# Performance work log

Measured on AMD Instinct MI355X. Metric: run time of the kernel, lower is better.

The kernel has to match this reference:

```python
import jax, jax.numpy as jnp
import numpy as np

D_AU, D_LM, D_GZ = 35, 196, 2   # au = 235 - 196 - 2 - 2
D, H = 128, 4
HD = D // H
LN_EPS = 1e-5


def setup_inputs() -> dict:
    key = jax.random.key(0)
    ks = jax.random.split(key, 12)
    s = lambda k, shape: jax.random.normal(k, shape, jnp.float32) * 0.02
    return {
        "video_feat": jax.random.normal(ks[0], (32, 4096, 235), jnp.float32),
        "au_w": s(ks[1], (D, D_AU)), "au_b": jnp.zeros((D,), jnp.float32),
        "lm_w": s(ks[2], (D, D_LM)), "lm_b": jnp.zeros((D,), jnp.float32),
        "gz_w": s(ks[3], (D, D_GZ)), "gz_b": jnp.zeros((D,), jnp.float32),
        "in_w": s(ks[4], (3 * D, D)), "in_b": jnp.zeros((3 * D,), jnp.float32),
        "out_w": s(ks[5], (D, D)), "out_b": jnp.zeros((D,), jnp.float32),
        "ln_g": jnp.ones((D,), jnp.float32), "ln_b": jnp.zeros((D,), jnp.float32),
        "w_w": s(ks[6], (1, D)), "w_b": jnp.zeros((1,), jnp.float32),
    }


def reference(video_feat, au_w, au_b, lm_w, lm_b, gz_w, gz_b,
              in_w, in_b, out_w, out_b, ln_g, ln_b, w_w, w_b):
    B, N, _ = video_feat.shape
    # split OpenFace3 features into semantic groups (meta dims unused, as in torch)
    au = video_feat[..., :D_AU]
    lm = video_feat[..., D_AU:D_AU + D_LM]
    gz = video_feat[..., D_AU + D_LM:D_AU + D_LM + D_GZ]
    au_h = au @ au_w.T + au_b
    lm_h = lm @ lm_w.T + lm_b
    gz_h = gz @ gz_w.T + gz_b
    tok = jnp.stack([au_h, lm_h, gz_h], axis=2).reshape(B * N, 3, D)  # (BN,3,D)

    # nn.MultiheadAttention (batch_first): packed in_proj then out_proj
    qkv = tok @ in_w.T + in_b                      # (BN,3,3D)
    q, k, v = jnp.split(qkv, 3, axis=-1)
    def heads(x):
        return x.reshape(-1, 3, H, HD).transpose(0, 2, 1, 3)  # (BN,H,3,HD)
    q, k, v = heads(q), heads(k), heads(v)
    scores = jnp.einsum('bhqd,bhkd->bhqk', q, k) / jnp.sqrt(jnp.float32(HD))
    attn = jax.nn.softmax(scores, axis=-1)
    o = jnp.einsum('bhqk,bhkd->bhqd', attn, v)
    o = o.transpose(0, 2, 1, 3).reshape(-1, 3, D)
    attn_out = o @ out_w.T + out_b

    # residual + LayerNorm
    x = attn_out + tok
    mu = x.mean(axis=-1, keepdims=True)
    var = x.var(axis=-1, keepdims=True)
    x = (x - mu) * jax.lax.rsqrt(var + LN_EPS) * ln_g + ln_b

    # softmax-weighted pooling over the 3 group tokens
    w = jax.nn.softmax((x @ w_w.T + w_b)[..., 0], axis=-1)  # (BN,3)
    fused = jnp.einsum('bt,btd->bd', w, x)
    return fused.reshape(B, N, D)
```

## Files before the change

### kernel.cpp

```cpp
#include <hip/hip_runtime.h>
#include <hip/hip_bf16.h>

typedef __hip_bfloat16 bf16;
typedef short  frag_t __attribute__((ext_vector_type(8)));
typedef float  f4     __attribute__((ext_vector_type(4)));
typedef unsigned short us8 __attribute__((ext_vector_type(8)));
typedef unsigned short us4 __attribute__((ext_vector_type(4)));

#define NPOS (32 * 4096)
#define CIN  235

#define W1F 0
#define W2F 98304
#define W3F 147456
#define FRAG_TOTAL 163840
#define FP32_OFF_BYTES (FRAG_TOTAL * 2)
#define F_BIAS 0
#define F_INB  384
#define F_OUTB 768
#define F_LNG  896
#define F_LNB  1024
#define F_GW   1152
#define F_BW   1280
#define F_SGW  1281
#define WS2_BYTES (FP32_OFF_BYTES + 1282 * 4)

__device__ __forceinline__ float b2f(bf16 x) { return __bfloat162float(x); }
__device__ __forceinline__ unsigned short f2b(float v) {
    bf16 h = __float2bfloat16(v);
    return __builtin_bit_cast(unsigned short, h);
}
__device__ __forceinline__ float b2fr(unsigned short u) {
    return __bfloat162float(__builtin_bit_cast(bf16, u));
}
__device__ __forceinline__ bool probe_is_f32(const void* ln_g) {
    return *(const unsigned int*)ln_g == 0x3F800000u;
}
__device__ __forceinline__ float ldany(const void* p, int i, bool f32) {
    return f32 ? ((const float*)p)[i] : b2f(((const bf16*)p)[i]);
}
template<typename IT> __device__ __forceinline__ float ldv(const void* p, size_t i);
template<> __device__ __forceinline__ float ldv<float>(const void* p, size_t i) { return ((const float*)p)[i]; }
template<> __device__ __forceinline__ float ldv<bf16>(const void* p, size_t i)  { return b2f(((const bf16*)p)[i]); }
template<typename IT> __device__ __forceinline__ void stv(void* p, size_t i, float v);
template<> __device__ __forceinline__ void stv<float>(void* p, size_t i, float v) { ((float*)p)[i] = v; }
template<> __device__ __forceinline__ void stv<bf16>(void* p, size_t i, float v)  { ((bf16*)p)[i] = __float2bfloat16(v); }

__device__ __forceinline__ int tok_idx(int row, int col) {
    return row * 128 + (col ^ ((row & 7) << 3));
}
__device__ __forceinline__ int qk_idx(int row, int col) {
    return row * 264 + col;
}
__device__ __forceinline__ int sx_idx(int row, int col) {
    return row * 132 + col;
}

__global__ __launch_bounds__(256) void kprep(
    const void* __restrict__ au_w, const void* __restrict__ au_b,
    const void* __restrict__ lm_w, const void* __restrict__ lm_b,
    const void* __restrict__ gz_w, const void* __restrict__ gz_b,
    const void* __restrict__ in_w, const void* __restrict__ in_b,
    const void* __restrict__ out_w, const void* __restrict__ out_b,
    const void* __restrict__ ln_g, const void* __restrict__ ln_b,
    const void* __restrict__ w_w, const void* __restrict__ w_b,
    void* __restrict__ ws)
{
    const bool f32 = probe_is_f32(ln_g);
    unsigned short* wf = (unsigned short*)ws;
    float* wsf = (float*)((char*)ws + FP32_OFF_BYTES);

    if (blockIdx.x == 645) {
        if (threadIdx.x < 64) {
            int lane = threadIdx.x;
            float bw = 0.f, sg = 0.f;
            for (int j = lane; j < 128; j += 64) {
                float wwj = ldany(w_w, j, f32);
                bw += ldany(ln_b, j, f32) * wwj;
                sg += ldany(ln_g, j, f32) * wwj;
            }
#pragma unroll
            for (int off = 32; off >= 1; off >>= 1) {
                bw += __shfl_down(bw, off);
                sg += __shfl_down(sg, off);
            }
            if (lane == 0) {
                wsf[F_BW]  = bw + ldany(w_b, 0, f32);
                wsf[F_SGW] = sg;
            }
        }
        return;
    }

    int idx = blockIdx.x * 256 + threadIdx.x;
    if (idx < FRAG_TOTAL) {
        float val = 0.f;
        if (idx < W2F) {
            int r = idx, j = r & 7, lane = (r >> 3) & 63, q = r >> 9;
            int tn = q % 24, ks = q / 24;
            int k = ks * 32 + (lane >> 4) * 8 + j;
            int c = tn * 16 + (lane & 15);
            int t = c >> 7, jo = c & 127;
            if (t == 0 && k < 35)                   val = ldany(au_w, jo * 35 + k, f32);
            else if (t == 1 && k >= 35 && k < 231)  val = ldany(lm_w, jo * 196 + (k - 35), f32);
            else if (t == 2 && k >= 231 && k < 233) val = ldany(gz_w, jo * 2 + (k - 231), f32);
        } else if (idx < W3F) {
            int r = idx - W2F, j = r & 7, lane = (r >> 3) & 63, q = r >> 9;
            int tn = q % 24, ks = q / 24;
            int k = ks * 32 + (lane >> 4) * 8 + j;
            int c = tn * 16 + (lane & 15);
            val = ldany(in_w, c * 128 + k, f32);
        } else {
            int r = idx - W3F, j = r & 7, lane = (r >> 3) & 63, q = r >> 9;
            int tn = q & 7, ks = q >> 3;
            int k = ks * 32 + (lane >> 4) * 8 + j;
            int c = tn * 16 + (lane & 15);
            val = ldany(out_w, c * 128 + k, f32);
        }
        wf[idx] = f2b(val);
    } else if (idx < FRAG_TOTAL + 1280) {
        int i2 = idx - FRAG_TOTAL;
        float v;
        if (i2 < 384) {
            int t = i2 >> 7, jo = i2 & 127;
            const void* b = (t == 0) ? au_b : ((t == 1) ? lm_b : gz_b);
            v = ldany(b, jo, f32);
        } else if (i2 < 768)  v = ldany(in_b,  i2 - 384, f32);
        else if   (i2 < 896)  v = ldany(out_b, i2 - 768, f32);
        else if   (i2 < 1024) v = ldany(ln_g,  i2 - 896, f32);
        else if   (i2 < 1152) v = ldany(ln_b,  i2 - 1024, f32);
        else                  v = ldany(ln_g, i2 - 1152, f32) * ldany(w_w, i2 - 1152, f32);
        wsf[i2] = v;
    }
}

__global__ __launch_bounds__(256, 4) void sga_mfma(
    const void* __restrict__ vf, const void* __restrict__ ln_g,
    const void* __restrict__ ws, void* __restrict__ out)
{
    const bool f32 = probe_is_f32(ln_g);
    const int tid = threadIdx.x;
    const int w = tid >> 6, lane = tid & 63, quad = lane >> 4, l16 = lane & 15;
    const int p0 = blockIdx.x * 16;

    const frag_t* wfr = (const frag_t*)ws;
    const float*  wsf = (const float*)((const char*)ws + FP32_OFF_BYTES);

    __shared__ __align__(16) unsigned char u_buf[25344];
    __shared__ __align__(16) unsigned short s_tok[6144];
    __shared__ float s_ar[576];
    __shared__ float s_mu[48], s_rs[48], s_w[16][3];

    unsigned short (*s_vf)[264] = (unsigned short(*)[264])u_buf;
    unsigned short* s_qkf = (unsigned short*)u_buf;
    float*          s_xf  = (float*)u_buf;

    for (int z = tid; z < 384; z += 256) {
        int rz = z / 24, cz = z - rz * 24;
        s_vf[rz][233 + cz] = 0;
    }
    if (f32) {
        const float* src = (const float*)vf + (size_t)p0 * CIN;
#pragma unroll
        for (int it = 0; it < 4; ++it) {
            int idx = it * 256 + tid;
            if (idx < 940) {
                float4 vv = *(const float4*)(src + idx * 4);
                int e = idx * 4;
                int r = e / 235, c = e - r * 235;
#pragma unroll
                for (int j = 0; j < 4; ++j) {
                    int rj = r, cj = c + j;
                    if (cj >= 235) { rj++; cj -= 235; }
                    if (cj < 233) s_vf[rj][cj] = f2b(((const float*)&vv)[j]);
                }
            }
        }
    } else {
        const unsigned short* src = (const unsigned short*)vf + (size_t)p0 * CIN;
#pragma unroll
        for (int it = 0; it < 2; ++it) {
            int idx = it * 256 + tid;
            if (idx < 470) {
                us8 vv = *(const us8*)(src + idx * 8);
                int e = idx * 8;
                int r = e / 235, c = e - r * 235;
#pragma unroll
                for (int j = 0; j < 8; ++j) {
                    int rj = r, cj = c + j;
                    if (cj >= 235) { rj++; cj -= 235; }
                    if (cj < 233) s_vf[rj][cj] = vv[j];
                }
            }
        }
    }
    __syncthreads();

    {
        frag_t a[8];
#pragma unroll
        for (int ks = 0; ks < 8; ++ks)
            a[ks] = *(const frag_t*)&s_vf[l16][ks * 32 + quad * 8];
#pragma unroll
        for (int tn6 = 0; tn6 < 6; ++tn6) {
            int tn = w * 6 + tn6;
            f4 acc = {0.f, 0.f, 0.f, 0.f};
#pragma unroll
            for (int ks = 0; ks < 8; ++ks) {
                frag_t b = wfr[W1F / 8 + (ks * 24 + tn) * 64 + lane];
                acc = __builtin_amdgcn_mfma_f32_16x16x32_bf16(b, a[ks], acc, 0, 0, 0);
            }
            int c0 = tn * 16 + quad * 4;
            int t = c0 >> 7, jo0 = c0 & 127;
            float4 bias = *(const float4*)&wsf[F_BIAS + c0];
            us4 pv;
            pv[0] = f2b(acc[0] + bias.x); pv[1] = f2b(acc[1] + bias.y);
            pv[2] = f2b(acc[2] + bias.z); pv[3] = f2b(acc[3] + bias.w);
            *(us4*)&s_tok[tok_idx(l16 * 3 + t, jo0)] = pv;
        }
    }
    __syncthreads();

    {
        frag_t a[3][4];
#pragma unroll
        for (int rt = 0; rt < 3; ++rt)
#pragma unroll
            for (int ks = 0; ks < 4; ++ks)
                a[rt][ks] = *(const frag_t*)&s_tok[tok_idx(rt * 16 + l16, ks * 32 + quad * 8)];
#pragma unroll
        for (int tn4 = 0; tn4 < 4; ++tn4) {
            int tn = w * 4 + tn4;
            f4 acc[3];
#pragma unroll
            for (int rt = 0; rt < 3; ++rt) acc[rt] = (f4){0.f, 0.f, 0.f, 0.f};
#pragma unroll
            for (int ks = 0; ks < 4; ++ks) {
                frag_t b = wfr[W2F / 8 + (ks * 24 + tn) * 64 + lane];
#pragma unroll
                for (int rt = 0; rt < 3; ++rt)
                    acc[rt] = __builtin_amdgcn_mfma_f32_16x16x32_bf16(b, a[rt][ks], acc[rt], 0, 0, 0);
            }
            int c0 = tn * 16 + quad * 4;
            float4 bias = *(const float4*)&wsf[F_INB + c0];
#pragma unroll
            for (int rt = 0; rt < 3; ++rt) {
                us4 pv;
                pv[0] = f2b(acc[rt][0] + bias.x); pv[1] = f2b(acc[rt][1] + bias.y);
                pv[2] = f2b(acc[rt][2] + bias.z); pv[3] = f2b(acc[rt][3] + bias.w);
                *(us4*)&s_qkf[qk_idx(rt * 16 + l16, c0)] = pv;
            }
        }
    }
    __syncthreads();

    {
        const int h = w;
        frag_t qf[3], kf[3];
#pragma unroll
        for (int t = 0; t < 3; ++t) {
            qf[t] = *(const frag_t*)&s_qkf[qk_idx(l16 * 3 + t, h * 32 + quad * 8)];
            kf[t] = *(const frag_t*)&s_qkf[qk_idx(l16 * 3 + t, 128 + h * 32 + quad * 8)];
        }
        float dv[3][3];
        const int rr = l16 & 3;
#pragma unroll
        for (int t = 0; t < 3; ++t)
#pragma unroll
            for (int k = 0; k < 3; ++k) {
                f4 acc = {0.f, 0.f, 0.f, 0.f};
                acc = __builtin_amdgcn_mfma_f32_16x16x32_bf16(qf[t], kf[k], acc, 0, 0, 0);
                float d = acc[0];
                d = rr == 1 ? acc[1] : d;
                d = rr == 2 ? acc[2] : d;
                d = rr == 3 ? acc[3] : d;
                dv[t][k] = d;
            }
        if ((l16 >> 2) == quad) {
            const float scale = 0.17677669529663687f;
            int base0 = (l16 * 4 + h) * 9;
#pragma unroll
            for (int t = 0; t < 3; ++t) {
                float s0 = dv[t][0] * scale, s1 = dv[t][1] * scale, s2 = dv[t][2] * scale;
                float m = fmaxf(s0, fmaxf(s1, s2));
                float e0 = __expf(s0 - m), e1 = __expf(s1 - m), e2 = __expf(s2 - m);
                float inv = 1.f / (e0 + e1 + e2);
                s_ar[base0 + t * 3 + 0] = e0 * inv;
                s_ar[base0 + t * 3 + 1] = e1 * inv;
                s_ar[base0 + t * 3 + 2] = e2 * inv;
            }
        }
    }
    __syncthreads();

    {
        frag_t a[3][4];
#pragma unroll
        for (int rt = 0; rt < 3; ++rt)
#pragma unroll
            for (int ks = 0; ks < 4; ++ks)
                a[rt][ks] = *(const frag_t*)&s_tok[tok_idx(rt * 16 + l16, ks * 32 + quad * 8)];
#pragma unroll
        for (int tn2 = 0; tn2 < 2; ++tn2) {
            int tn = 16 + w * 2 + tn2;
            f4 acc[3];
#pragma unroll
            for (int rt = 0; rt < 3; ++rt) acc[rt] = (f4){0.f, 0.f, 0.f, 0.f};
#pragma unroll
            for (int ks = 0; ks < 4; ++ks) {
                frag_t b = wfr[W2F / 8 + (ks * 24 + tn) * 64 + lane];
#pragma unroll
                for (int rt = 0; rt < 3; ++rt)
                    acc[rt] = __builtin_amdgcn_mfma_f32_16x16x32_bf16(b, a[rt][ks], acc[rt], 0, 0, 0);
            }
            int c0 = tn * 16 + quad * 4;
            float4 bias = *(const float4*)&wsf[F_INB + c0];
#pragma unroll
            for (int rt = 0; rt < 3; ++rt) {
                us4 pv;
                pv[0] = f2b(acc[rt][0] + bias.x); pv[1] = f2b(acc[rt][1] + bias.y);
                pv[2] = f2b(acc[rt][2] + bias.z); pv[3] = f2b(acc[rt][3] + bias.w);
                *(us4*)&s_qkf[qk_idx(rt * 16 + l16, c0 - 256)] = pv;
            }
        }
    }
    __syncthreads();

    for (int u = 0; u < 3; ++u) {
        int unit = u * 256 + tid;
        int row = unit >> 4, c8 = (unit & 15) << 3;
        int p = row / 3, t = row - p * 3, h = c8 >> 5;
        int base = (p * 4 + h) * 9 + t * 3;
        float a0 = s_ar[base], a1 = s_ar[base + 1], a2 = s_ar[base + 2];
        us8 v0 = *(const us8*)&s_qkf[qk_idx(p * 3 + 0, c8)];
        us8 v1 = *(const us8*)&s_qkf[qk_idx(p * 3 + 1, c8)];
        us8 v2 = *(const us8*)&s_qkf[qk_idx(p * 3 + 2, c8)];
        us8 o;
#pragma unroll
        for (int jj = 0; jj < 8; ++jj)
            o[jj] = f2b(a0 * b2fr(v0[jj]) + a1 * b2fr(v1[jj]) + a2 * b2fr(v2[jj]));
        *(us8*)&s_qkf[qk_idx(row, 128 + c8)] = o;
    }
    __syncthreads();

    frag_t of[3][4];
#pragma unroll
    for (int rt = 0; rt < 3; ++rt)
#pragma unroll
        for (int ks = 0; ks < 4; ++ks)
            of[rt][ks] = *(const frag_t*)&s_qkf[qk_idx(rt * 16 + l16, 128 + ks * 32 + quad * 8)];
    __syncthreads();

    {
#pragma unroll
        for (int tn2 = 0; tn2 < 2; ++tn2) {
            int tn = w * 2 + tn2;
            f4 acc[3];
#pragma unroll
            for (int rt = 0; rt < 3; ++rt) acc[rt] = (f4){0.f, 0.f, 0.f, 0.f};
#pragma unroll
            for (int ks = 0; ks < 4; ++ks) {
                frag_t b = wfr[W3F / 8 + (ks * 8 + tn) * 64 + lane];
#pragma unroll
                for (int rt = 0; rt < 3; ++rt)
                    acc[rt] = __builtin_amdgcn_mfma_f32_16x16x32_bf16(b, of[rt][ks], acc[rt], 0, 0, 0);
            }
            int c0 = tn * 16 + quad * 4;
            float4 ob4 = *(const float4*)&wsf[F_OUTB + c0];
#pragma unroll
            for (int rt = 0; rt < 3; ++rt) {
                int row = rt * 16 + l16;
                us4 tv = *(const us4*)&s_tok[tok_idx(row, c0)];
                float4 xv;
                xv.x = acc[rt][0] + ob4.x + b2fr(tv[0]);
                xv.y = acc[rt][1] + ob4.y + b2fr(tv[1]);
                xv.z = acc[rt][2] + ob4.z + b2fr(tv[2]);
                xv.w = acc[rt][3] + ob4.w + b2fr(tv[3]);
                *(float4*)&s_xf[sx_idx(row, c0)] = xv;
            }
        }
    }
    __syncthreads();

    if (tid < 192) {
        int row = tid >> 2, part = tid & 3;
        float s = 0.f, ss = 0.f, sg = 0.f;
#pragma unroll
        for (int cc = 0; cc < 8; ++cc) {
            float4 xv = *(const float4*)&s_xf[sx_idx(row, part * 32 + cc * 4)];
            int cg = F_GW + part * 32 + cc * 4;
            s  += xv.x + xv.y + xv.z + xv.w;
            ss += xv.x * xv.x + xv.y * xv.y + xv.z * xv.z + xv.w * xv.w;
            sg += xv.x * wsf[cg] + xv.y * wsf[cg + 1] + xv.z * wsf[cg + 2] + xv.w * wsf[cg + 3];
        }
        int b = (row * 4 + part) * 3;
        s_ar[b] = s; s_ar[b + 1] = ss; s_ar[b + 2] = sg;
    }
    __syncthreads();
    if (tid < 64) {
        float lg = 0.f;
        if (lane < 48) {
            float s = 0.f, ss = 0.f, sg = 0.f;
#pragma unroll
            for (int part = 0; part < 4; ++part) {
                int b = (lane * 4 + part) * 3;
                s += s_ar[b]; ss += s_ar[b + 1]; sg += s_ar[b + 2];
            }
            float mu  = s * (1.f / 128.f);
            float var = ss * (1.f / 128.f) - mu * mu;
            float rs  = rsqrtf(var + 1e-5f);
            s_mu[lane] = mu; s_rs[lane] = rs;
            lg = wsf[F_BW] + rs * (sg - mu * wsf[F_SGW]);
        }
        float l0 = __shfl(lg, 3 * lane);
        float l1 = __shfl(lg, 3 * lane + 1);
        float l2 = __shfl(lg, 3 * lane + 2);
        if (lane < 16) {
            float m = fmaxf(l0, fmaxf(l1, l2));
            float e0 = __expf(l0 - m), e1 = __expf(l1 - m), e2 = __expf(l2 - m);
            float inv = 1.f / (e0 + e1 + e2);
            s_w[lane][0] = e0 * inv; s_w[lane][1] = e1 * inv; s_w[lane][2] = e2 * inv;
        }
    }
    __syncthreads();

    {
#pragma unroll
        for (int it = 0; it < 2; ++it) {
            int task = it * 256 + tid;
            int p = task >> 5, cg = (task & 31) * 4;
            int row0 = p * 3;
            float c0 = s_w[p][0] * s_rs[row0];
            float c1 = s_w[p][1] * s_rs[row0 + 1];
            float c2 = s_w[p][2] * s_rs[row0 + 2];
            float C  = c0 * s_mu[row0] + c1 * s_mu[row0 + 1] + c2 * s_mu[row0 + 2];
            float4 g = *(const float4*)&wsf[F_LNG + cg];
            float4 b = *(const float4*)&wsf[F_LNB + cg];
            float4 x0 = *(const float4*)&s_xf[sx_idx(row0, cg)];
            float4 x1 = *(const float4*)&s_xf[sx_idx(row0 + 1, cg)];
            float4 x2 = *(const float4*)&s_xf[sx_idx(row0 + 2, cg)];
            float4 f;
            f.x = (c0 * x0.x + c1 * x1.x + c2 * x2.x - C) * g.x + b.x;
            f.y = (c0 * x0.y + c1 * x1.y + c2 * x2.y - C) * g.y + b.y;
            f.z = (c0 * x0.z + c1 * x1.z + c2 * x2.z - C) * g.z + b.z;
            f.w = (c0 * x0.w + c1 * x1.w + c2 * x2.w - C) * g.w + b.w;
            size_t o0 = (size_t)(p0 + p) * 128 + cg;
            if (f32) {
                *(float4*)((float*)out + o0) = f;
            } else {
                us4 pv;
                pv[0] = f2b(f.x); pv[1] = f2b(f.y); pv[2] = f2b(f.z); pv[3] = f2b(f.w);
                *(us4*)((bf16*)out + o0) = pv;
            }
        }
    }
}

#define P 4
struct SmemFB {
    float vf[P][233];
    alignas(16) float tok[P][128][4];
    float qkv[P][3][384];
    float att[P][4][3][3];
    alignas(16) float o[P][128][4];
    float x[P][3][128];
    float red[P][3][2];
    float w[P][4];
};

template<typename IT>
__device__ void sga_fb_body(SmemFB& s,
    const void* vf, const void* au_w, const void* au_b, const void* lm_w,
    const void* lm_b, const void* gz_w, const void* gz_b, const void* in_w,
    const void* in_b, const void* out_w, const void* out_b, const void* ln_g,
    const void* ln_b, const void* w_w, const void* w_b, void* out)
{
    const int j = threadIdx.x;
    const int p0 = blockIdx.x * P;
    for (int p = 0; p < P; ++p) {
        size_t rb = (size_t)(p0 + p) * CIN;
        for (int d = j; d < 233; d += 128) s.vf[p][d] = ldv<IT>(vf, rb + d);
    }
    __syncthreads();
    {
        float a_au[P], a_lm[P], a_gz[P];
        const float bau = ldv<IT>(au_b, j), blm = ldv<IT>(lm_b, j), bgz = ldv<IT>(gz_b, j);
#pragma unroll
        for (int p = 0; p < P; ++p) { a_au[p] = bau; a_lm[p] = blm; a_gz[p] = bgz; }
        for (int d = 0; d < 35; ++d) {
            float w = ldv<IT>(au_w, j * 35 + d);
#pragma unroll
            for (int p = 0; p < P; ++p) a_au[p] += s.vf[p][d] * w;
        }
        for (int d = 0; d < 196; ++d) {
            float w = ldv<IT>(lm_w, j * 196 + d);
#pragma unroll
            for (int p = 0; p < P; ++p) a_lm[p] += s.vf[p][35 + d] * w;
        }
        for (int d = 0; d < 2; ++d) {
            float w = ldv<IT>(gz_w, j * 2 + d);
#pragma unroll
            for (int p = 0; p < P; ++p) a_gz[p] += s.vf[p][231 + d] * w;
        }
#pragma unroll
        for (int p = 0; p < P; ++p) {
            s.tok[p][j][0] = a_au[p]; s.tok[p][j][1] = a_lm[p];
            s.tok[p][j][2] = a_gz[p]; s.tok[p][j][3] = 0.f;
        }
    }
    __syncthreads();
    {
        float acc[P][3][3];
#pragma unroll
        for (int rr = 0; rr < 3; ++rr) {
            float b = ldv<IT>(in_b, j + rr * 128);
#pragma unroll
            for (int p = 0; p < P; ++p)
#pragma unroll
                for (int t = 0; t < 3; ++t) acc[p][rr][t] = b;
        }
        for (int d = 0; d < 128; ++d) {
            const float w0 = ldv<IT>(in_w, (j)       * 128 + d);
            const float w1 = ldv<IT>(in_w, (j + 128) * 128 + d);
            const float w2 = ldv<IT>(in_w, (j + 256) * 128 + d);
#pragma unroll
            for (int p = 0; p < P; ++p) {
                const float4 tv = *(const float4*)&s.tok[p][d][0];
                acc[p][0][0] += tv.x * w0; acc[p][0][1] += tv.y * w0; acc[p][0][2] += tv.z * w0;
                acc[p][1][0] += tv.x * w1; acc[p][1][1] += tv.y * w1; acc[p][1][2] += tv.z * w1;
                acc[p][2][0] += tv.x * w2; acc[p][2][1] += tv.y * w2; acc[p][2][2] += tv.z * w2;
            }
        }
#pragma unroll
        for (int p = 0; p < P; ++p)
#pragma unroll
            for (int rr = 0; rr < 3; ++rr)
#pragma unroll
                for (int t = 0; t < 3; ++t)
                    s.qkv[p][t][j + rr * 128] = acc[p][rr][t];
    }
    __syncthreads();
    for (int i = j; i < P * 36; i += 128) {
        int p = i / 36, r = i % 36, h = r / 9, t = (r / 3) % 3, k = r % 3;
        const float* qp = &s.qkv[p][t][h * 32];
        const float* kp = &s.qkv[p][k][128 + h * 32];
        float sc = 0.f;
#pragma unroll
        for (int d = 0; d < 32; ++d) sc += qp[d] * kp[d];
        s.att[p][h][t][k] = sc * 0.17677669529663687f;
    }
    __syncthreads();
    if (j < P * 12) {
        int p = j / 12, r = j % 12, h = r / 3, t = r % 3;
        float l0 = s.att[p][h][t][0], l1 = s.att[p][h][t][1], l2 = s.att[p][h][t][2];
        float m = fmaxf(l0, fmaxf(l1, l2));
        float e0 = __expf(l0 - m), e1 = __expf(l1 - m), e2 = __expf(l2 - m);
        float inv = 1.f / (e0 + e1 + e2);
        s.att[p][h][t][0] = e0 * inv; s.att[p][h][t][1] = e1 * inv; s.att[p][h][t][2] = e2 * inv;
    }
    __syncthreads();
    {
        const int h = j >> 5;
#pragma unroll
        for (int p = 0; p < P; ++p) {
            const float v0 = s.qkv[p][0][256 + j];
            const float v1 = s.qkv[p][1][256 + j];
            const float v2 = s.qkv[p][2][256 + j];
#pragma unroll
            for (int t = 0; t < 3; ++t)
                s.o[p][j][t] = s.att[p][h][t][0] * v0 + s.att[p][h][t][1] * v1
                             + s.att[p][h][t][2] * v2;
            s.o[p][j][3] = 0.f;
        }
    }
    __syncthreads();
    {
        float acc[P][3];
        const float ob = ldv<IT>(out_b, j);
#pragma unroll
        for (int p = 0; p < P; ++p)
#pragma unroll
            for (int t = 0; t < 3; ++t) acc[p][t] = ob;
        for (int d = 0; d < 128; ++d) {
            const float w = ldv<IT>(out_w, j * 128 + d);
#pragma unroll
            for (int p = 0; p < P; ++p) {
                const float4 ov = *(const float4*)&s.o[p][d][0];
                acc[p][0] += ov.x * w; acc[p][1] += ov.y * w; acc[p][2] += ov.z * w;
            }
        }
#pragma unroll
        for (int p = 0; p < P; ++p)
#pragma unroll
            for (int t = 0; t < 3; ++t)
                s.x[p][t][j] = acc[p][t] + s.tok[p][j][t];
    }
    __syncthreads();
    if (j < P * 3) {
        int p = j / 3, t = j % 3;
        float sm = 0.f, ss = 0.f;
        for (int d = 0; d < 128; ++d) { float v = s.x[p][t][d]; sm += v; ss += v * v; }
        float mu = sm * (1.f / 128.f);
        float var = ss * (1.f / 128.f) - mu * mu;
        s.red[p][t][0] = mu; s.red[p][t][1] = rsqrtf(var + 1e-5f);
    }
    __syncthreads();
    {
        const float g = ldv<IT>(ln_g, j), b = ldv<IT>(ln_b, j);
#pragma unroll
        for (int p = 0; p < P; ++p)
#pragma unroll
            for (int t = 0; t < 3; ++t) {
                float mu = s.red[p][t][0], rs = s.red[p][t][1];
                s.x[p][t][j] = (s.x[p][t][j] - mu) * rs * g + b;
            }
    }
    __syncthreads();
    if (j < P * 3) {
        int p = j / 3, t = j % 3;
        float lg = ldv<IT>(w_b, 0);
        for (int d = 0; d < 128; ++d) lg += s.x[p][t][d] * ldv<IT>(w_w, d);
        s.red[p][t][0] = lg;
    }
    __syncthreads();
    if (j < P) {
        float l0 = s.red[j][0][0], l1 = s.red[j][1][0], l2 = s.red[j][2][0];
        float m = fmaxf(l0, fmaxf(l1, l2));
        float e0 = __expf(l0 - m), e1 = __expf(l1 - m), e2 = __expf(l2 - m);
        float inv = 1.f / (e0 + e1 + e2);
        s.w[j][0] = e0 * inv; s.w[j][1] = e1 * inv; s.w[j][2] = e2 * inv;
    }
    __syncthreads();
#pragma unroll
    for (int p = 0; p < P; ++p) {
        float f = s.w[p][0] * s.x[p][0][j] + s.w[p][1] * s.x[p][1][j]
                + s.w[p][2] * s.x[p][2][j];
        stv<IT>(out, (size_t)(p0 + p) * 128 + j, f);
    }
}

__global__ __launch_bounds__(128) void sga_fb(
    const void* vf, const void* au_w, const void* au_b, const void* lm_w,
    const void* lm_b, const void* gz_w, const void* gz_b, const void* in_w,
    const void* in_b, const void* out_w, const void* out_b, const void* ln_g,
    const void* ln_b, const void* w_w, const void* w_b, void* out)
{
    __shared__ SmemFB s;
    if (probe_is_f32(ln_g))
        sga_fb_body<float>(s, vf, au_w, au_b, lm_w, lm_b, gz_w, gz_b, in_w, in_b,
                           out_w, out_b, ln_g, ln_b, w_w, w_b, out);
    else
        sga_fb_body<bf16>(s, vf, au_w, au_b, lm_w, lm_b, gz_w, gz_b, in_w, in_b,
                          out_w, out_b, ln_g, ln_b, w_w, w_b, out);
}

extern "C" void kernel_launch(void* const* d_in, const int* in_sizes, int n_in,
                              void* d_out, int out_size, void* d_ws, size_t ws_size,
                              hipStream_t stream) {
    const void* vf    = d_in[0];
    const void* au_w  = d_in[1];
    const void* au_b  = d_in[2];
    const void* lm_w  = d_in[3];
    const void* lm_b  = d_in[4];
    const void* gz_w  = d_in[5];
    const void* gz_b  = d_in[6];
    const void* in_w  = d_in[7];
    const void* in_b  = d_in[8];
    const void* out_w = d_in[9];
    const void* out_b = d_in[10];
    const void* ln_g  = d_in[11];
    const void* ln_b  = d_in[12];
    const void* w_w   = d_in[13];
    const void* w_b   = d_in[14];

    if (ws_size >= (size_t)WS2_BYTES) {
        kprep<<<646, 256, 0, stream>>>(au_w, au_b, lm_w, lm_b, gz_w, gz_b,
                                       in_w, in_b, out_w, out_b, ln_g, ln_b,
                                       w_w, w_b, d_ws);
        sga_mfma<<<NPOS / 16, 256, 0, stream>>>(vf, ln_g, d_ws, d_out);
    } else {
        sga_fb<<<NPOS / P, 128, 0, stream>>>(vf, au_w, au_b, lm_w, lm_b, gz_w,
                                             gz_b, in_w, in_b, out_w, out_b,
                                             ln_g, ln_b, w_w, w_b, d_out);
    }
}
```

Before: 354.4 us.

## Use 512-thread blocks in MFMA kernel, splitting per-wave tile work in half

Doubles the block size of the fused MFMA kernel from 256 to 512 threads (8 waves) and halves the number of output tiles each wave computes in every GEMM stage, attention score stage and elementwise stage. The aim is more waves per block to hide LDS and global latency and shorten the serial per-wave chains between barriers. In exchange, the launch bound of 512x8 caps registers per thread. Each block still uses the same shared memory, so fewer blocks may fit per CU, and barriers now synchronise more waves.

After: 350.6 us. No clear change (-1.1%).

```diff
diff --git a/kernel.cpp b/kernel.cpp
--- a/kernel.cpp
+++ b/kernel.cpp
@@ -134,7 +134,7 @@
     }
 }
 
-__global__ __launch_bounds__(256, 4) void sga_mfma(
+__global__ __launch_bounds__(512, 8) void sga_mfma(
     const void* __restrict__ vf, const void* __restrict__ ln_g,
     const void* __restrict__ ws, void* __restrict__ out)
 {
@@ -155,15 +155,15 @@
     unsigned short* s_qkf = (unsigned short*)u_buf;
     float*          s_xf  = (float*)u_buf;
 
-    for (int z = tid; z < 384; z += 256) {
-        int rz = z / 24, cz = z - rz * 24;
+    if (tid < 384) {
+        int rz = tid / 24, cz = tid - rz * 24;
         s_vf[rz][233 + cz] = 0;
     }
     if (f32) {
         const float* src = (const float*)vf + (size_t)p0 * CIN;
 #pragma unroll
-        for (int it = 0; it < 4; ++it) {
-            int idx = it * 256 + tid;
+        for (int it = 0; it < 2; ++it) {
+            int idx = it * 512 + tid;
             if (idx < 940) {
                 float4 vv = *(const float4*)(src + idx * 4);
                 int e = idx * 4;
@@ -178,19 +178,15 @@
         }
     } else {
         const unsigned short* src = (const unsigned short*)vf + (size_t)p0 * CIN;
-#pragma unroll
-        for (int it = 0; it < 2; ++it) {
-            int idx = it * 256 + tid;
-            if (idx < 470) {
-                us8 vv = *(const us8*)(src + idx * 8);
-                int e = idx * 8;
-                int r = e / 235, c = e - r * 235;
-#pragma unroll
-                for (int j = 0; j < 8; ++j) {
-                    int rj = r, cj = c + j;
-                    if (cj >= 235) { rj++; cj -= 235; }
-                    if (cj < 233) s_vf[rj][cj] = vv[j];
-                }
+        if (tid < 470) {
+            us8 vv = *(const us8*)(src + tid * 8);
+            int e = tid * 8;
+            int r = e / 235, c = e - r * 235;
+#pragma unroll
+            for (int j = 0; j < 8; ++j) {
+                int rj = r, cj = c + j;
+                if (cj >= 235) { rj++; cj -= 235; }
+                if (cj < 233) s_vf[rj][cj] = vv[j];
             }
         }
     }
@@ -202,8 +198,8 @@
         for (int ks = 0; ks < 8; ++ks)
             a[ks] = *(const frag_t*)&s_vf[l16][ks * 32 + quad * 8];
 #pragma unroll
-        for (int tn6 = 0; tn6 < 6; ++tn6) {
-            int tn = w * 6 + tn6;
+        for (int tn3 = 0; tn3 < 3; ++tn3) {
+            int tn = w * 3 + tn3;
             f4 acc = {0.f, 0.f, 0.f, 0.f};
 #pragma unroll
             for (int ks = 0; ks < 8; ++ks) {
@@ -229,8 +225,8 @@
             for (int ks = 0; ks < 4; ++ks)
                 a[rt][ks] = *(const frag_t*)&s_tok[tok_idx(rt * 16 + l16, ks * 32 + quad * 8)];
 #pragma unroll
-        for (int tn4 = 0; tn4 < 4; ++tn4) {
-            int tn = w * 4 + tn4;
+        for (int tn2 = 0; tn2 < 2; ++tn2) {
+            int tn = w * 2 + tn2;
             f4 acc[3];
 #pragma unroll
             for (int rt = 0; rt < 3; ++rt) acc[rt] = (f4){0.f, 0.f, 0.f, 0.f};
@@ -255,39 +251,37 @@
     __syncthreads();
 
     {
-        const int h = w;
-        frag_t qf[3], kf[3];
-#pragma unroll
-        for (int t = 0; t < 3; ++t) {
-            qf[t] = *(const frag_t*)&s_qkf[qk_idx(l16 * 3 + t, h * 32 + quad * 8)];
-            kf[t] = *(const frag_t*)&s_qkf[qk_idx(l16 * 3 + t, 128 + h * 32 + quad * 8)];
-        }
-        float dv[3][3];
+        const int h = w >> 1;
+        const int t0 = (w & 1) ? 2 : 0, t1 = (w & 1) ? 3 : 2;
+        frag_t kf[3];
+#pragma unroll
+        for (int k = 0; k < 3; ++k)
+            kf[k] = *(const frag_t*)&s_qkf[qk_idx(l16 * 3 + k, 128 + h * 32 + quad * 8)];
         const int rr = l16 & 3;
-#pragma unroll
-        for (int t = 0; t < 3; ++t)
+        const bool diag = (l16 >> 2) == quad;
+        const float scale = 0.17677669529663687f;
+        for (int t = t0; t < t1; ++t) {
+            frag_t qf = *(const frag_t*)&s_qkf[qk_idx(l16 * 3 + t, h * 32 + quad * 8)];
+            float dv[3];
 #pragma unroll
             for (int k = 0; k < 3; ++k) {
                 f4 acc = {0.f, 0.f, 0.f, 0.f};
-                acc = __builtin_amdgcn_mfma_f32_16x16x32_bf16(qf[t], kf[k], acc, 0, 0, 0);
+                acc = __builtin_amdgcn_mfma_f32_16x16x32_bf16(qf, kf[k], acc, 0, 0, 0);
                 float d = acc[0];
                 d = rr == 1 ? acc[1] : d;
                 d = rr == 2 ? acc[2] : d;
                 d = rr == 3 ? acc[3] : d;
-                dv[t][k] = d;
-            }
-        if ((l16 >> 2) == quad) {
-            const float scale = 0.17677669529663687f;
-            int base0 = (l16 * 4 + h) * 9;
-#pragma unroll
-            for (int t = 0; t < 3; ++t) {
-                float s0 = dv[t][0] * scale, s1 = dv[t][1] * scale, s2 = dv[t][2] * scale;
+                dv[k] = d;
+            }
+            if (diag) {
+                float s0 = dv[0] * scale, s1 = dv[1] * scale, s2 = dv[2] * scale;
                 float m = fmaxf(s0, fmaxf(s1, s2));
                 float e0 = __expf(s0 - m), e1 = __expf(s1 - m), e2 = __expf(s2 - m);
                 float inv = 1.f / (e0 + e1 + e2);
-                s_ar[base0 + t * 3 + 0] = e0 * inv;
-                s_ar[base0 + t * 3 + 1] = e1 * inv;
-                s_ar[base0 + t * 3 + 2] = e2 * inv;
+                int base0 = (l16 * 4 + h) * 9 + t * 3;
+                s_ar[base0 + 0] = e0 * inv;
+                s_ar[base0 + 1] = e1 * inv;
+                s_ar[base0 + 2] = e2 * inv;
             }
         }
     }
@@ -300,9 +294,8 @@
 #pragma unroll
             for (int ks = 0; ks < 4; ++ks)
                 a[rt][ks] = *(const frag_t*)&s_tok[tok_idx(rt * 16 + l16, ks * 32 + quad * 8)];
-#pragma unroll
-        for (int tn2 = 0; tn2 < 2; ++tn2) {
-            int tn = 16 + w * 2 + tn2;
+        {
+            int tn = 16 + w;
             f4 acc[3];
 #pragma unroll
             for (int rt = 0; rt < 3; ++rt) acc[rt] = (f4){0.f, 0.f, 0.f, 0.f};
@@ -326,20 +319,23 @@
     }
     __syncthreads();
 
-    for (int u = 0; u < 3; ++u) {
-        int unit = u * 256 + tid;
-        int row = unit >> 4, c8 = (unit & 15) << 3;
-        int p = row / 3, t = row - p * 3, h = c8 >> 5;
-        int base = (p * 4 + h) * 9 + t * 3;
-        float a0 = s_ar[base], a1 = s_ar[base + 1], a2 = s_ar[base + 2];
-        us8 v0 = *(const us8*)&s_qkf[qk_idx(p * 3 + 0, c8)];
-        us8 v1 = *(const us8*)&s_qkf[qk_idx(p * 3 + 1, c8)];
-        us8 v2 = *(const us8*)&s_qkf[qk_idx(p * 3 + 2, c8)];
-        us8 o;
-#pragma unroll
-        for (int jj = 0; jj < 8; ++jj)
-            o[jj] = f2b(a0 * b2fr(v0[jj]) + a1 * b2fr(v1[jj]) + a2 * b2fr(v2[jj]));
-        *(us8*)&s_qkf[qk_idx(row, 128 + c8)] = o;
+#pragma unroll
+    for (int u = 0; u < 2; ++u) {
+        int unit = u * 512 + tid;
+        if (unit < 768) {
+            int row = unit >> 4, c8 = (unit & 15) << 3;
+            int p = row / 3, t = row - p * 3, h = c8 >> 5;
+            int base = (p * 4 + h) * 9 + t * 3;
+            float a0 = s_ar[base], a1 = s_ar[base + 1], a2 = s_ar[base + 2];
+            us8 v0 = *(const us8*)&s_qkf[qk_idx(p * 3 + 0, c8)];
+            us8 v1 = *(const us8*)&s_qkf[qk_idx(p * 3 + 1, c8)];
+            us8 v2 = *(const us8*)&s_qkf[qk_idx(p * 3 + 2, c8)];
+            us8 o;
+#pragma unroll
+            for (int jj = 0; jj < 8; ++jj)
+                o[jj] = f2b(a0 * b2fr(v0[jj]) + a1 * b2fr(v1[jj]) + a2 * b2fr(v2[jj]));
+            *(us8*)&s_qkf[qk_idx(row, 128 + c8)] = o;
+        }
     }
     __syncthreads();
 
@@ -352,32 +348,29 @@
     __syncthreads();
 
     {
-#pragma unroll
-        for (int tn2 = 0; tn2 < 2; ++tn2) {
-            int tn = w * 2 + tn2;
-            f4 acc[3];
-#pragma unroll
-            for (int rt = 0; rt < 3; ++rt) acc[rt] = (f4){0.f, 0.f, 0.f, 0.f};
-#pragma unroll
-            for (int ks = 0; ks < 4; ++ks) {
-                frag_t b = wfr[W3F / 8 + (ks * 8 + tn) * 64 + lane];
-#pragma unroll
-                for (int rt = 0; rt < 3; ++rt)
-                    acc[rt] = __builtin_amdgcn_mfma_f32_16x16x32_bf16(b, of[rt][ks], acc[rt], 0, 0, 0);
-            }
-            int c0 = tn * 16 + quad * 4;
-            float4 ob4 = *(const float4*)&wsf[F_OUTB + c0];
-#pragma unroll
-            for (int rt = 0; rt < 3; ++rt) {
-                int row = rt * 16 + l16;
-                us4 tv = *(const us4*)&s_tok[tok_idx(row, c0)];
-                float4 xv;
-                xv.x = acc[rt][0] + ob4.x + b2fr(tv[0]);
-                xv.y = acc[rt][1] + ob4.y + b2fr(tv[1]);
-                xv.z = acc[rt][2] + ob4.z + b2fr(tv[2]);
-                xv.w = acc[rt][3] + ob4.w + b2fr(tv[3]);
-                *(float4*)&s_xf[sx_idx(row, c0)] = xv;
-            }
+        int tn = w;
+        f4 acc[3];
+#pragma unroll
+        for (int rt = 0; rt < 3; ++rt) acc[rt] = (f4){0.f, 0.f, 0.f, 0.f};
+#pragma unroll
+        for (int ks = 0; ks < 4; ++ks) {
+            frag_t b = wfr[W3F / 8 + (ks * 8 + tn) * 64 + lane];
+#pragma unroll
+            for (int rt = 0; rt < 3; ++rt)
+                acc[rt] = __builtin_amdgcn_mfma_f32_16x16x32_bf16(b, of[rt][ks], acc[rt], 0, 0, 0);
+        }
+        int c0 = tn * 16 + quad * 4;
+        float4 ob4 = *(const float4*)&wsf[F_OUTB + c0];
+#pragma unroll
+        for (int rt = 0; rt < 3; ++rt) {
+            int row = rt * 16 + l16;
+            us4 tv = *(const us4*)&s_tok[tok_idx(row, c0)];
+            float4 xv;
+            xv.x = acc[rt][0] + ob4.x + b2fr(tv[0]);
+            xv.y = acc[rt][1] + ob4.y + b2fr(tv[1]);
+            xv.z = acc[rt][2] + ob4.z + b2fr(tv[2]);
+            xv.w = acc[rt][3] + ob4.w + b2fr(tv[3]);
+            *(float4*)&s_xf[sx_idx(row, c0)] = xv;
         }
     }
     __syncthreads();
@@ -425,33 +418,29 @@
     __syncthreads();
 
     {
-#pragma unroll
-        for (int it = 0; it < 2; ++it) {
-            int task = it * 256 + tid;
-            int p = task >> 5, cg = (task & 31) * 4;
-            int row0 = p * 3;
-            float c0 = s_w[p][0] * s_rs[row0];
-            float c1 = s_w[p][1] * s_rs[row0 + 1];
-            float c2 = s_w[p][2] * s_rs[row0 + 2];
-            float C  = c0 * s_mu[row0] + c1 * s_mu[row0 + 1] + c2 * s_mu[row0 + 2];
-            float4 g = *(const float4*)&wsf[F_LNG + cg];
-            float4 b = *(const float4*)&wsf[F_LNB + cg];
-            float4 x0 = *(const float4*)&s_xf[sx_idx(row0, cg)];
-            float4 x1 = *(const float4*)&s_xf[sx_idx(row0 + 1, cg)];
-            float4 x2 = *(const float4*)&s_xf[sx_idx(row0 + 2, cg)];
-            float4 f;
-            f.x = (c0 * x0.x + c1 * x1.x + c2 * x2.x - C) * g.x + b.x;
-            f.y = (c0 * x0.y + c1 * x1.y + c2 * x2.y - C) * g.y + b.y;
-            f.z = (c0 * x0.z + c1 * x1.z + c2 * x2.z - C) * g.z + b.z;
-            f.w = (c0 * x0.w + c1 * x1.w + c2 * x2.w - C) * g.w + b.w;
-            size_t o0 = (size_t)(p0 + p) * 128 + cg;
-            if (f32) {
-                *(float4*)((float*)out + o0) = f;
-            } else {
-                us4 pv;
-                pv[0] = f2b(f.x); pv[1] = f2b(f.y); pv[2] = f2b(f.z); pv[3] = f2b(f.w);
-                *(us4*)((bf16*)out + o0) = pv;
-            }
+        int p = tid >> 5, cg = (tid & 31) * 4;
+        int row0 = p * 3;
+        float c0 = s_w[p][0] * s_rs[row0];
+        float c1 = s_w[p][1] * s_rs[row0 + 1];
+        float c2 = s_w[p][2] * s_rs[row0 + 2];
+        float C  = c0 * s_mu[row0] + c1 * s_mu[row0 + 1] + c2 * s_mu[row0 + 2];
+        float4 g = *(const float4*)&wsf[F_LNG + cg];
+        float4 b = *(const float4*)&wsf[F_LNB + cg];
+        float4 x0 = *(const float4*)&s_xf[sx_idx(row0, cg)];
+        float4 x1 = *(const float4*)&s_xf[sx_idx(row0 + 1, cg)];
+        float4 x2 = *(const float4*)&s_xf[sx_idx(row0 + 2, cg)];
+        float4 f;
+        f.x = (c0 * x0.x + c1 * x1.x + c2 * x2.x - C) * g.x + b.x;
+        f.y = (c0 * x0.y + c1 * x1.y + c2 * x2.y - C) * g.y + b.y;
+        f.z = (c0 * x0.z + c1 * x1.z + c2 * x2.z - C) * g.z + b.z;
+        f.w = (c0 * x0.w + c1 * x1.w + c2 * x2.w - C) * g.w + b.w;
+        size_t o0 = (size_t)(p0 + p) * 128 + cg;
+        if (f32) {
+            *(float4*)((float*)out + o0) = f;
+        } else {
+            us4 pv;
+            pv[0] = f2b(f.x); pv[1] = f2b(f.y); pv[2] = f2b(f.z); pv[3] = f2b(f.w);
+            *(us4*)((bf16*)out + o0) = pv;
         }
     }
 }
@@ -677,7 +666,7 @@
         kprep<<<646, 256, 0, stream>>>(au_w, au_b, lm_w, lm_b, gz_w, gz_b,
                                        in_w, in_b, out_w, out_b, ln_g, ln_b,
                                        w_w, w_b, d_ws);
-        sga_mfma<<<NPOS / 16, 256, 0, stream>>>(vf, ln_g, d_ws, d_out);
+        sga_mfma<<<NPOS / 16, 512, 0, stream>>>(vf, ln_g, d_ws, d_out);
     } else {
         sga_fb<<<NPOS / P, 128, 0, stream>>>(vf, au_w, au_b, lm_w, lm_b, gz_w,
                                              gz_b, in_w, in_b, out_w, out_b,
```
